# Kernel tuning notes

Measured on AMD Instinct MI355X. Metric: run time of the kernel, lower is better.

The kernel has to match this reference:

```python
import jax, jax.numpy as jnp
import numpy as np

B, S, DIM, HEADS, DHEAD = 1, 1992, 2048, 16, 128
NKI_SEQ_ALIGN = 128
EPS = 1e-6


def setup_inputs() -> dict:
    key = jax.random.key(0)
    ks = jax.random.split(key, 8)
    hidden_states = jax.random.normal(ks[0], (B, S, DIM), dtype=jnp.float32)
    # realistic rotary tables, full head_dim with interleaved pair angles
    pos = jnp.arange(S, dtype=jnp.float32)
    inv_freq = 1.0 / (10000.0 ** (jnp.arange(0, DHEAD, 2, dtype=jnp.float32) / DHEAD))
    ang = pos[:, None] * inv_freq[None, :]                      # [S, DHEAD/2]
    full = jnp.stack([ang, ang], axis=-1).reshape(S, DHEAD)     # interleave
    freqs_cos = jnp.cos(full)[None, :, None, :]                 # [1,S,1,DHEAD]
    freqs_sin = jnp.sin(full)[None, :, None, :]
    sc = 0.02
    wq = jax.random.normal(ks[1], (DIM, DIM), dtype=jnp.float32) * sc
    wk = jax.random.normal(ks[2], (DIM, DIM), dtype=jnp.float32) * sc
    wv = jax.random.normal(ks[3], (DIM, DIM), dtype=jnp.float32) * sc
    wo = jax.random.normal(ks[4], (DIM, DIM), dtype=jnp.float32) * sc
    bq = jax.random.normal(ks[5], (DIM,), dtype=jnp.float32) * sc
    bk = jax.random.normal(ks[6], (DIM,), dtype=jnp.float32) * sc
    bv = jax.random.normal(ks[7], (DIM,), dtype=jnp.float32) * sc
    bo = jnp.zeros((DIM,), dtype=jnp.float32)
    norm_q_w = jnp.ones((DIM,), dtype=jnp.float32)
    norm_k_w = jnp.ones((DIM,), dtype=jnp.float32)
    return dict(hidden_states=hidden_states, freqs_cos=freqs_cos, freqs_sin=freqs_sin,
                wq=wq, bq=bq, wk=wk, bk=bk, wv=wv, bv=bv,
                norm_q_w=norm_q_w, norm_k_w=norm_k_w, wo=wo, bo=bo)


def _rms_norm(x, weight, eps=EPS):
    xf = x.astype(jnp.float32)
    var = jnp.mean(xf * xf, axis=-1, keepdims=True)
    return (weight * (xf * jax.lax.rsqrt(var + eps))).astype(x.dtype)


def _apply_rope(x, freqs_cos, freqs_sin):
    # x: [B,H,S,D]; freqs: [1,S,1,D]
    cos = jnp.transpose(freqs_cos[..., 0::2], (0, 2, 1, 3))  # [1,1,S,D/2]
    sin = jnp.transpose(freqs_sin[..., 1::2], (0, 2, 1, 3))
    x1, x2 = x[..., 0::2], x[..., 1::2]
    o1 = x1 * cos - x2 * sin
    o2 = x1 * sin + x2 * cos
    return jnp.stack([o1, o2], axis=-1).reshape(x.shape)


def _attention_padded(q, k, v):
    # Faithful to nki_flash_attention: zero-pad seq to multiple of 128,
    # no masking of padded keys (they contribute logit 0), trim query pad.
    B_, H_, S_, D_ = q.shape
    pad = (-S_) % NKI_SEQ_ALIGN
    if pad:
        pc = [(0, 0), (0, 0), (0, pad), (0, 0)]
        q = jnp.pad(q, pc); k = jnp.pad(k, pc); v = jnp.pad(v, pc)
    scale = 1.0 / np.sqrt(D_)
    scores = jnp.einsum('bhqd,bhkd->bhqk', q, k) * scale
    probs = jax.nn.softmax(scores, axis=-1)
    out = jnp.einsum('bhqk,bhkd->bhqd', probs, v)
    return out[:, :, :S_, :]


def reference(hidden_states, freqs_cos, freqs_sin, wq, bq, wk, bk, wv, bv,
              norm_q_w, norm_k_w, wo, bo):
    b, s, _ = hidden_states.shape
    q = hidden_states @ wq.T + bq
    k = hidden_states @ wk.T + bk
    v = hidden_states @ wv.T + bv
    q = _rms_norm(q, norm_q_w)
    k = _rms_norm(k, norm_k_w)
    hd = q.shape[-1] // HEADS
    q = q.reshape(b, s, HEADS, hd).transpose(0, 2, 1, 3)
    k = k.reshape(b, s, HEADS, hd).transpose(0, 2, 1, 3)
    v = v.reshape(b, s, HEADS, hd).transpose(0, 2, 1, 3)
    q = _apply_rope(q, freqs_cos, freqs_sin)
    k = _apply_rope(k, freqs_cos, freqs_sin)
    o = _attention_padded(q, k, v)
    o = o.transpose(0, 2, 1, 3).reshape(b, s, -1)
    return o @ wo.T + bo
```

## Files before the change

kernel.cpp:

```cpp
#include <hip/hip_runtime.h>
#include <cstdint>

#define S_REAL 1992
#define S_PAD  2048
#define DIMSZ  2048
#define NHEAD  16
#define DHD    128

typedef float f32x4 __attribute__((ext_vector_type(4)));
typedef float f32x16 __attribute__((ext_vector_type(16)));
typedef __bf16 bf16x8 __attribute__((ext_vector_type(8)));
typedef unsigned short u16x8 __attribute__((ext_vector_type(8)));

__device__ __forceinline__ unsigned short f2bf(float f){
  uint32_t u = __float_as_uint(f);
  u += 0x7fffu + ((u >> 16) & 1u);
  return (unsigned short)(u >> 16);
}

__device__ __forceinline__ void gload16(const void* g, void* l){
  __builtin_amdgcn_global_load_lds(
      (const __attribute__((address_space(1))) uint32_t*)g,
      (__attribute__((address_space(3))) uint32_t*)l,
      16, 0, 0);
}

__launch_bounds__(256)
__global__ void k_cvt5(const float* __restrict__ s0, const float* __restrict__ s1,
                       const float* __restrict__ s2, const float* __restrict__ s3,
                       const float* __restrict__ s4,
                       unsigned short* __restrict__ d0, unsigned short* __restrict__ d1,
                       unsigned short* __restrict__ d2, unsigned short* __restrict__ d3,
                       unsigned short* __restrict__ d4,
                       int nX, int nW)
{
  int i = blockIdx.x * 256 + threadIdx.x;
  const float* s; unsigned short* d; int j;
  if (i < nX){ s = s0; d = d0; j = i; }
  else {
    int k = i - nX;
    int wsel = k / nW; j = k - wsel * nW;
    s = (wsel == 0) ? s1 : (wsel == 1) ? s2 : (wsel == 2) ? s3 : s4;
    d = (wsel == 0) ? d1 : (wsel == 1) ? d2 : (wsel == 2) ? d3 : d4;
  }
  const float4* sp = (const float4*)s + (size_t)j * 2;
  float4 a = sp[0], b = sp[1];
  u16x8 o;
  o[0]=f2bf(a.x); o[1]=f2bf(a.y); o[2]=f2bf(a.z); o[3]=f2bf(a.w);
  o[4]=f2bf(b.x); o[5]=f2bf(b.y); o[6]=f2bf(b.z); o[7]=f2bf(b.w);
  *((u16x8*)d + j) = o;
}

template<int BN>
__launch_bounds__(256, 2)
__global__ void k_g64(const unsigned short* __restrict__ A,
                      const unsigned short* __restrict__ B0,
                      const unsigned short* __restrict__ B1,
                      const unsigned short* __restrict__ B2,
                      const float* __restrict__ bias0,
                      const float* __restrict__ bias1,
                      const float* __restrict__ bias2,
                      float* __restrict__ C0, float* __restrict__ C1,
                      unsigned short* __restrict__ Cb,
                      int Mreal)
{
  constexpr int WN   = (BN == 128) ? 2 : 1;
  constexpr int WM   = 4 / WN;
  constexpr int MB   = (128 / WM) / 32;
  constexpr int NB   = (BN / WN) / 32;
  constexpr int AE   = 128 * 64;
  constexpr int BE   = BN * 64;
  constexpr int BUFE = AE + BE;
  constexpr int NT   = DIMSZ / 64;
  constexpr int TN   = DIMSZ / BN;
  __shared__ unsigned short lds[2 * BUFE];

  const unsigned short* Bm = (blockIdx.z == 0) ? B0 : ((blockIdx.z == 1) ? B1 : B2);
  const float* bias        = (blockIdx.z == 0) ? bias0 : ((blockIdx.z == 1) ? bias1 : bias2);
  float* C                 = (blockIdx.z == 0) ? C0 : C1;

  const int fid = blockIdx.x + gridDim.x * blockIdx.y;
  const int q   = (gridDim.x * gridDim.y) >> 3;
  const int nf  = (fid & 7) * q + (fid >> 3);
  const int m0  = (nf / TN) * 128, n0 = (nf % TN) * BN;

  const int tid = threadIdx.x;
  const int w = tid >> 6, l = tid & 63;
  const int l31 = l & 31, l5 = l >> 5;
  const int wr = (w / WN) * (128 / WM);
  const int wc = (w % WN) * (BN / WN);

  f32x16 acc[MB][NB];
  #pragma unroll
  for (int mb = 0; mb < MB; ++mb)
    #pragma unroll
    for (int nb = 0; nb < NB; ++nb)
      #pragma unroll
      for (int r = 0; r < 16; ++r) acc[mb][nb][r] = 0.f;

#define G64_STAGE(TT, PP) do{                                                     \
    const int k0s = (TT) * 64;                                                    \
    unsigned short* dst = &lds[(PP) * BUFE];                                      \
    _Pragma("unroll")                                                             \
    for (int i_ = 0; i_ < AE / 2048; ++i_){                                       \
      int lin = i_ * 256 + tid;                                                   \
      int r_ = lin >> 3, sl_ = lin & 7;                                           \
      int gr_ = m0 + r_; if (gr_ > Mreal - 1) gr_ = Mreal - 1;                    \
      gload16(A + (size_t)gr_ * DIMSZ + k0s + (sl_ ^ (r_ & 7)) * 8,               \
              dst + lin * 8);                                                     \
    }                                                                             \
    _Pragma("unroll")                                                             \
    for (int i_ = 0; i_ < BE / 2048; ++i_){                                       \
      int lin = i_ * 256 + tid;                                                   \
      int r_ = lin >> 3, sl_ = lin & 7;                                           \
      gload16(Bm + (size_t)(n0 + r_) * DIMSZ + k0s + (sl_ ^ (r_ & 7)) * 8,        \
              dst + AE + lin * 8);                                                \
    }                                                                             \
  } while(0)

#define G64_COMPUTE(PP) do{                                                       \
    const unsigned short* sb = &lds[(PP) * BUFE];                                 \
    bf16x8 a_[MB][4], b_[NB][4];                                                  \
    _Pragma("unroll")                                                             \
    for (int mb = 0; mb < MB; ++mb)                                               \
      _Pragma("unroll")                                                           \
      for (int ks = 0; ks < 4; ++ks){                                             \
        int r_ = wr + mb * 32 + l31;                                              \
        int c_ = (ks * 2 + l5) ^ (r_ & 7);                                        \
        a_[mb][ks] = *(const bf16x8*)(sb + r_ * 64 + c_ * 8);                     \
      }                                                                           \
    _Pragma("unroll")                                                             \
    for (int nb = 0; nb < NB; ++nb)                                               \
      _Pragma("unroll")                                                           \
      for (int ks = 0; ks < 4; ++ks){                                             \
        int r_ = wc + nb * 32 + l31;                                              \
        int c_ = (ks * 2 + l5) ^ (r_ & 7);                                        \
        b_[nb][ks] = *(const bf16x8*)(sb + AE + r_ * 64 + c_ * 8);                \
      }                                                                           \
    __builtin_amdgcn_s_setprio(1);                                                \
    _Pragma("unroll")                                                             \
    for (int ks = 0; ks < 4; ++ks)                                                \
      _Pragma("unroll")                                                           \
      for (int mb = 0; mb < MB; ++mb)                                             \
        _Pragma("unroll")                                                         \
        for (int nb = 0; nb < NB; ++nb)                                           \
          acc[mb][nb] = __builtin_amdgcn_mfma_f32_32x32x16_bf16(a_[mb][ks],       \
                            b_[nb][ks], acc[mb][nb], 0, 0, 0);                    \
    __builtin_amdgcn_s_setprio(0);                                                \
  } while(0)

  G64_STAGE(0, 0);
  asm volatile("s_waitcnt vmcnt(0)" ::: "memory");
  __builtin_amdgcn_s_barrier();
  int p = 0;
  for (int tt = 0; tt < NT; ++tt){
    if (tt + 1 < NT) G64_STAGE(tt + 1, p ^ 1);
    G64_COMPUTE(p);
    asm volatile("s_waitcnt vmcnt(0)" ::: "memory");
    __builtin_amdgcn_s_barrier();
    p ^= 1;
  }
#undef G64_STAGE
#undef G64_COMPUTE

  const bool vout = (blockIdx.z == 2);
  #pragma unroll
  for (int nb = 0; nb < NB; ++nb){
    int col = n0 + wc + nb * 32 + l31;
    float bz = bias[col];
    #pragma unroll
    for (int mb = 0; mb < MB; ++mb){
      #pragma unroll
      for (int r = 0; r < 16; ++r){
        int row = m0 + wr + mb * 32 + (r & 3) + 8 * (r >> 2) + 4 * l5;
        if (row < Mreal){
          if (vout) Cb[(size_t)row * DIMSZ + col] = f2bf(acc[mb][nb][r] + bz);
          else      C[(size_t)row * DIMSZ + col] = acc[mb][nb][r] + bz;
        }
      }
    }
  }
}

__launch_bounds__(256)
__global__ void k_normrope2(const float* __restrict__ Qf, const float* __restrict__ Kf,
                            const float* __restrict__ nqw, const float* __restrict__ nkw,
                            const float* __restrict__ fc, const float* __restrict__ fs,
                            unsigned short* __restrict__ OutQ, unsigned short* __restrict__ OutK)
{
  const int s = blockIdx.x;
  const int isK = blockIdx.y;
  const float* Xf = isK ? Kf : Qf;
  const float* nw = isK ? nkw : nqw;
  unsigned short* Out = isK ? OutK : OutQ;
  const float scale = isK ? 1.0f : (0.08838834764831843f * 1.4426950408889634f);
  const int swz = isK;

  const int t = threadIdx.x;
  const int w = t >> 6, l = t & 63;
  __shared__ float wred[4];
  float v[8];
  float ss = 0.f;
  if (s < S_REAL){
    const float4* p = (const float4*)(Xf + (size_t)s * DIMSZ) + t * 2;
    float4 a = p[0], b = p[1];
    v[0]=a.x; v[1]=a.y; v[2]=a.z; v[3]=a.w; v[4]=b.x; v[5]=b.y; v[6]=b.z; v[7]=b.w;
    #pragma unroll
    for (int j = 0; j < 8; ++j) ss += v[j] * v[j];
  }
  #pragma unroll
  for (int off = 32; off >= 1; off >>= 1) ss += __shfl_xor(ss, off);
  if (l == 0) wred[w] = ss;
  __syncthreads();
  float tot = wred[0] + wred[1] + wred[2] + wred[3];
  float rinv = rsqrtf(tot * (1.f / DIMSZ) + 1e-6f);

  const int h  = t >> 4;
  const int d0 = (t & 15) * 8;
  const int b  = t & 15;
  const int bsw = swz ? (b ^ (s & 7)) : b;
  unsigned short* dst = Out + ((size_t)h * S_PAD + s) * DHD + bsw * 8;
  u16x8 o;
  if (s < S_REAL){
    #pragma unroll
    for (int i = 0; i < 4; ++i){
      float c_ = fc[s * DHD + d0 + 2 * i];
      float s_ = fs[s * DHD + d0 + 2 * i + 1];
      float x1 = v[2 * i]     * rinv * nw[t * 8 + 2 * i];
      float x2 = v[2 * i + 1] * rinv * nw[t * 8 + 2 * i + 1];
      o[2 * i]     = f2bf((x1 * c_ - x2 * s_) * scale);
      o[2 * i + 1] = f2bf((x1 * s_ + x2 * c_) * scale);
    }
  } else {
    #pragma unroll
    for (int j = 0; j < 8; ++j) o[j] = 0;
  }
  *(u16x8*)dst = o;
}

__launch_bounds__(256)
__global__ void k_vtrans(const unsigned short* __restrict__ Vb, unsigned short* __restrict__ Vth)
{
  __shared__ unsigned short tile[64][72];
  const int t = threadIdx.x;
  const int s0 = blockIdx.x * 64, c0 = blockIdx.y * 64;
  #pragma unroll
  for (int i = 0; i < 2; ++i){
    int lin = i * 256 + t;
    int r = lin >> 3, ck = lin & 7;
    u16x8 val = (u16x8){0,0,0,0,0,0,0,0};
    if (s0 + r < S_REAL)
      val = *(const u16x8*)(Vb + (size_t)(s0 + r) * DIMSZ + c0 + ck * 8);
    *(u16x8*)&tile[r][ck * 8] = val;
  }
  __syncthreads();
  const int cl = t >> 2;
  const int cc = c0 + cl;
  #pragma unroll
  for (int bi = 0; bi < 2; ++bi){
    int b = (t & 3) * 2 + bi;
    u16x8 o;
    #pragma unroll
    for (int j = 0; j < 8; ++j) o[j] = tile[b * 8 + j][cl];
    int bsw = b ^ (cc & 7);
    *(u16x8*)(Vth + (size_t)cc * S_PAD + s0 + bsw * 8) = o;
  }
}

__launch_bounds__(512)
__global__ void k_attn(const unsigned short* __restrict__ Qh,
                       const unsigned short* __restrict__ Kh,
                       const unsigned short* __restrict__ Vth,
                       unsigned short* __restrict__ O)
{
  __shared__ unsigned short kbuf[3][64 * 128];
  __shared__ unsigned short vbuf[4][128 * 64];
  __shared__ unsigned short pbuf[8][16 * 64];
  const int flat = blockIdx.x + gridDim.x * blockIdx.y;
  const int h  = (flat & 7) * 2 + ((flat >> 3) & 1);
  const int q0 = (flat >> 4) * 128;
  const int t = threadIdx.x, w = t >> 6, l = t & 63;
  const int lr = l & 15, lg = l >> 4;

  const unsigned short* Qp = Qh + ((size_t)h * S_PAD + q0 + w * 16 + lr) * DHD;
  bf16x8 qf[4];
  #pragma unroll
  for (int ks = 0; ks < 4; ++ks) qf[ks] = *(const bf16x8*)(Qp + ks * 32 + lg * 8);

  f32x4 acc[8];
  #pragma unroll
  for (int nf = 0; nf < 8; ++nf) acc[nf] = (f32x4){0.f, 0.f, 0.f, 0.f};
  float m = -3.0e38f, lsum = 0.f;

#define ATT_STAGE(KT, BK_, BV_) do{                                                 \
    _Pragma("unroll")                                                               \
    for (int i_ = 0; i_ < 2; ++i_){                                                 \
      int lin = i_ * 512 + t;                                                       \
      int rK = lin >> 4, ckK = lin & 15;                                            \
      gload16(Kh + ((size_t)h * S_PAD + (KT) * 64 + rK) * DHD + ckK * 8,            \
              &kbuf[BK_][lin * 8]);                                                 \
    }                                                                               \
    _Pragma("unroll")                                                               \
    for (int i_ = 0; i_ < 2; ++i_){                                                 \
      int lin = i_ * 512 + t;                                                       \
      int rV = lin >> 3, ckV = lin & 7;                                             \
      gload16(Vth + ((size_t)h * DHD + rV) * S_PAD + (KT) * 64 + ckV * 8,           \
              &vbuf[BV_][lin * 8]);                                                 \
    }                                                                               \
  } while(0)

#define SM_PV(SF, VB) do{                                                           \
    float pmax = SF[0][0];                                                          \
    _Pragma("unroll")                                                               \
    for (int kvf = 0; kvf < 4; ++kvf)                                               \
      _Pragma("unroll")                                                             \
      for (int j = 0; j < 4; ++j) pmax = fmaxf(pmax, SF[kvf][j]);                   \
    pmax = fmaxf(pmax, __shfl_xor(pmax, 16));                                       \
    pmax = fmaxf(pmax, __shfl_xor(pmax, 32));                                       \
    float fr = 1.f;                                                                 \
    if (!__all(pmax - m <= 8.0f)){                                                  \
      float mn = fmaxf(m, pmax);                                                    \
      fr = exp2f(m - mn);                                                           \
      m = mn;                                                                       \
      float fv0 = __shfl(fr, lg * 4 + 0);                                           \
      float fv1 = __shfl(fr, lg * 4 + 1);                                           \
      float fv2 = __shfl(fr, lg * 4 + 2);                                           \
      float fv3 = __shfl(fr, lg * 4 + 3);                                           \
      f32x4 fv = (f32x4){fv0, fv1, fv2, fv3};                                       \
      _Pragma("unroll")                                                             \
      for (int nf = 0; nf < 8; ++nf) acc[nf] *= fv;                                 \
    }                                                                               \
    float p_[4][4];                                                                 \
    float psum = 0.f;                                                               \
    _Pragma("unroll")                                                               \
    for (int kvf = 0; kvf < 4; ++kvf)                                               \
      _Pragma("unroll")                                                             \
      for (int j = 0; j < 4; ++j){ p_[kvf][j] = exp2f(SF[kvf][j] - m); psum += p_[kvf][j]; } \
    lsum = lsum * fr + psum;                                                        \
    char* pb = (char*)pbuf[w];                                                      \
    _Pragma("unroll")                                                               \
    for (int kvf = 0; kvf < 4; ++kvf){                                              \
      uint2 wv;                                                                     \
      wv.x = (uint32_t)f2bf(p_[kvf][0]) | ((uint32_t)f2bf(p_[kvf][1]) << 16);       \
      wv.y = (uint32_t)f2bf(p_[kvf][2]) | ((uint32_t)f2bf(p_[kvf][3]) << 16);       \
      int byte = lr * 128 + (((kvf * 2 + (lg >> 1)) ^ (lr & 7)) * 16) + (lg & 1) * 8;\
      *(uint2*)(pb + byte) = wv;                                                    \
    }                                                                               \
    bf16x8 pf[2];                                                                   \
    _Pragma("unroll")                                                               \
    for (int c = 0; c < 2; ++c)                                                     \
      pf[c] = *(const bf16x8*)(pb + lr * 128 + ((c * 4 + lg) ^ (lr & 7)) * 16);     \
    __builtin_amdgcn_s_setprio(1);                                                  \
    _Pragma("unroll")                                                               \
    for (int nf = 0; nf < 8; ++nf){                                                 \
      int cc = nf * 16 + lr;                                                        \
      _Pragma("unroll")                                                             \
      for (int ks = 0; ks < 2; ++ks){                                               \
        int blk = (ks * 4 + lg) ^ (cc & 7);                                         \
        bf16x8 vf = *(const bf16x8*)&vbuf[VB][cc * 64 + blk * 8];                   \
        acc[nf] = __builtin_amdgcn_mfma_f32_16x16x32_bf16(pf[ks], vf, acc[nf], 0, 0, 0); \
      }                                                                             \
    }                                                                               \
    __builtin_amdgcn_s_setprio(0);                                                  \
  } while(0)

  ATT_STAGE(0, 0, 0);
  ATT_STAGE(1, 1, 1);
  asm volatile("s_waitcnt vmcnt(4)" ::: "memory");
  __builtin_amdgcn_s_barrier();

  constexpr int NKT = S_PAD / 64;
  f32x4 sfp[4];
  int kb = 0, sk = 2, sv = 2, vp = 3;
  for (int kt = 0; kt < NKT; ++kt){
    if (kt < NKT - 2) ATT_STAGE(kt + 2, sk, sv);

    f32x4 sfc[4];
    __builtin_amdgcn_s_setprio(1);
    #pragma unroll
    for (int kvf = 0; kvf < 4; ++kvf){
      sfc[kvf] = (f32x4){0.f, 0.f, 0.f, 0.f};
      int r = kvf * 16 + lr;
      #pragma unroll
      for (int ks = 0; ks < 4; ++ks){
        int blk = (ks * 4 + lg) ^ (r & 7);
        bf16x8 kf = *(const bf16x8*)&kbuf[kb][r * 128 + blk * 8];
        sfc[kvf] = __builtin_amdgcn_mfma_f32_16x16x32_bf16(kf, qf[ks], sfc[kvf], 0, 0, 0);
      }
    }
    __builtin_amdgcn_s_setprio(0);

    if (kt > 0) SM_PV(sfp, vp);

    #pragma unroll
    for (int kvf = 0; kvf < 4; ++kvf) sfp[kvf] = sfc[kvf];

    if (kt < NKT - 2)       asm volatile("s_waitcnt vmcnt(4)" ::: "memory");
    else if (kt == NKT - 2) asm volatile("s_waitcnt vmcnt(0)" ::: "memory");
    if (kt < NKT - 1) __builtin_amdgcn_s_barrier();

    kb = (kb == 2) ? 0 : kb + 1;
    sk = (sk == 2) ? 0 : sk + 1;
    sv = (sv == 3) ? 0 : sv + 1;
    vp = (vp == 3) ? 0 : vp + 1;
  }
  SM_PV(sfp, vp);
#undef ATT_STAGE
#undef SM_PV

  lsum += __shfl_xor(lsum, 16);
  lsum += __shfl_xor(lsum, 32);
  float ls0 = __shfl(lsum, lg * 4 + 0);
  float ls1 = __shfl(lsum, lg * 4 + 1);
  float ls2 = __shfl(lsum, lg * 4 + 2);
  float ls3 = __shfl(lsum, lg * 4 + 3);
  f32x4 lsv = (f32x4){1.f / ls0, 1.f / ls1, 1.f / ls2, 1.f / ls3};

  #pragma unroll
  for (int nf = 0; nf < 8; ++nf){
    #pragma unroll
    for (int j = 0; j < 4; ++j){
      int row = q0 + w * 16 + lg * 4 + j;
      if (row < S_REAL)
        O[(size_t)row * DIMSZ + h * DHD + nf * 16 + lr] = f2bf(acc[nf][j] * lsv[j]);
    }
  }
}

extern "C" void kernel_launch(void* const* d_in, const int* in_sizes, int n_in,
                              void* d_out, int out_size, void* d_ws, size_t ws_size,
                              hipStream_t stream)
{
  const float* hidden = (const float*)d_in[0];
  const float* fc  = (const float*)d_in[1];
  const float* fs  = (const float*)d_in[2];
  const float* wq  = (const float*)d_in[3];
  const float* bq  = (const float*)d_in[4];
  const float* wk  = (const float*)d_in[5];
  const float* bk  = (const float*)d_in[6];
  const float* wv  = (const float*)d_in[7];
  const float* bv  = (const float*)d_in[8];
  const float* nqw = (const float*)d_in[9];
  const float* nkw = (const float*)d_in[10];
  const float* wo  = (const float*)d_in[11];
  const float* bo  = (const float*)d_in[12];
  float* out = (float*)d_out;

  char* ws = (char*)d_ws;
  size_t off = 0;
  auto alloc = [&](size_t bytes) -> void* {
    void* p = ws + off;
    off += (bytes + 255) & ~(size_t)255;
    return p;
  };
  unsigned short* Xb  = (unsigned short*)alloc((size_t)S_REAL * DIMSZ * 2);
  unsigned short* Wqb = (unsigned short*)alloc((size_t)DIMSZ * DIMSZ * 2);
  unsigned short* Wkb = (unsigned short*)alloc((size_t)DIMSZ * DIMSZ * 2);
  unsigned short* Wvb = (unsigned short*)alloc((size_t)DIMSZ * DIMSZ * 2);
  unsigned short* Wob = (unsigned short*)alloc((size_t)DIMSZ * DIMSZ * 2);
  float* Qf = (float*)alloc((size_t)S_REAL * DIMSZ * 4);
  float* Kf = (float*)alloc((size_t)S_REAL * DIMSZ * 4);
  unsigned short* Vb  = (unsigned short*)alloc((size_t)S_REAL * DIMSZ * 2);
  unsigned short* Qhh = (unsigned short*)alloc((size_t)NHEAD * S_PAD * DHD * 2);
  unsigned short* Khh = (unsigned short*)alloc((size_t)NHEAD * S_PAD * DHD * 2);
  unsigned short* Vth = (unsigned short*)alloc((size_t)NHEAD * DHD * S_PAD * 2);
  unsigned short* Oa  = (unsigned short*)alloc((size_t)S_REAL * DIMSZ * 2);

  {
    int nX = S_REAL * DIMSZ / 8;
    int nW = DIMSZ * DIMSZ / 8;
    int total = nX + 4 * nW;
    k_cvt5<<<total / 256, 256, 0, stream>>>(hidden, wq, wk, wv, wo,
                                            Xb, Wqb, Wkb, Wvb, Wob, nX, nW);
  }

  k_g64<128><<<dim3(16, 16, 3), 256, 0, stream>>>(Xb, Wqb, Wkb, Wvb, bq, bk, bv,
                                                  Qf, Kf, Vb, S_REAL);

  k_normrope2<<<dim3(S_PAD, 2), 256, 0, stream>>>(Qf, Kf, nqw, nkw, fc, fs, Qhh, Khh);

  k_vtrans<<<dim3(S_PAD / 64, DIMSZ / 64), 256, 0, stream>>>(Vb, Vth);

  k_attn<<<dim3(S_PAD / 128, NHEAD), 512, 0, stream>>>(Qhh, Khh, Vth, Oa);

  k_g64<64><<<dim3(16, 32, 1), 256, 0, stream>>>(Oa, Wob, Wob, Wob, bo, bo, bo,
                                                 out, out, nullptr, S_REAL);
}
```

Measured before the change: 233.8 us.

## Switch GEMMs to triple-buffered K=32 pipeline and store Q/K as bf16

Replaces the double-buffered K=64 GEMM with a triple-buffered K=32 kernel that keeps two tile loads in flight. It waits with vmcnt(4) so the next stage's loads overlap compute, and the smaller LDS footprint allows three blocks per CU. Q and K projections are now written as bf16 instead of fp32, which halves the intermediate traffic read by the norm/rope kernel at some precision cost before RMS norm. The output projection now uses 128x128 tiles with 256 blocks instead of 128x64 tiles with 512.

```diff
diff --git a/kernel.cpp b/kernel.cpp
--- a/kernel.cpp
+++ b/kernel.cpp
@@ -18,11 +18,20 @@
   return (unsigned short)(u >> 16);
 }
 
+__device__ __forceinline__ float bf2f(unsigned short b){
+  return __uint_as_float((uint32_t)b << 16);
+}
+
 __device__ __forceinline__ void gload16(const void* g, void* l){
   __builtin_amdgcn_global_load_lds(
       (const __attribute__((address_space(1))) uint32_t*)g,
       (__attribute__((address_space(3))) uint32_t*)l,
       16, 0, 0);
+}
+
+template<int N> __device__ __forceinline__ void waitbar(){
+  if constexpr (N == 4) asm volatile("s_waitcnt vmcnt(4)\n\ts_barrier" ::: "memory");
+  else                  asm volatile("s_waitcnt vmcnt(0)\n\ts_barrier" ::: "memory");
 }
 
 __launch_bounds__(256)
@@ -51,131 +60,128 @@
   *((u16x8*)d + j) = o;
 }
 
-template<int BN>
-__launch_bounds__(256, 2)
-__global__ void k_g64(const unsigned short* __restrict__ A,
+__launch_bounds__(256, 3)
+__global__ void k_g32(const unsigned short* __restrict__ A,
                       const unsigned short* __restrict__ B0,
                       const unsigned short* __restrict__ B1,
                       const unsigned short* __restrict__ B2,
                       const float* __restrict__ bias0,
                       const float* __restrict__ bias1,
                       const float* __restrict__ bias2,
-                      float* __restrict__ C0, float* __restrict__ C1,
-                      unsigned short* __restrict__ Cb,
-                      int Mreal)
-{
-  constexpr int WN   = (BN == 128) ? 2 : 1;
-  constexpr int WM   = 4 / WN;
-  constexpr int MB   = (128 / WM) / 32;
-  constexpr int NB   = (BN / WN) / 32;
-  constexpr int AE   = 128 * 64;
-  constexpr int BE   = BN * 64;
-  constexpr int BUFE = AE + BE;
-  constexpr int NT   = DIMSZ / 64;
-  constexpr int TN   = DIMSZ / BN;
-  __shared__ unsigned short lds[2 * BUFE];
+                      float* __restrict__ C0,
+                      unsigned short* __restrict__ Cb0,
+                      unsigned short* __restrict__ Cb1,
+                      unsigned short* __restrict__ Cb2,
+                      int bf16_out, int Mreal)
+{
+  constexpr int BUFE = 8192;
+  constexpr int NT   = DIMSZ / 32;
+  __shared__ unsigned short lds[3 * BUFE];
 
   const unsigned short* Bm = (blockIdx.z == 0) ? B0 : ((blockIdx.z == 1) ? B1 : B2);
   const float* bias        = (blockIdx.z == 0) ? bias0 : ((blockIdx.z == 1) ? bias1 : bias2);
-  float* C                 = (blockIdx.z == 0) ? C0 : C1;
+  unsigned short* Cbm      = (blockIdx.z == 0) ? Cb0 : ((blockIdx.z == 1) ? Cb1 : Cb2);
 
   const int fid = blockIdx.x + gridDim.x * blockIdx.y;
   const int q   = (gridDim.x * gridDim.y) >> 3;
   const int nf  = (fid & 7) * q + (fid >> 3);
-  const int m0  = (nf / TN) * 128, n0 = (nf % TN) * BN;
+  const int m0  = (nf >> 4) * 128, n0 = (nf & 15) * 128;
 
   const int tid = threadIdx.x;
   const int w = tid >> 6, l = tid & 63;
   const int l31 = l & 31, l5 = l >> 5;
-  const int wr = (w / WN) * (128 / WM);
-  const int wc = (w % WN) * (BN / WN);
-
-  f32x16 acc[MB][NB];
-  #pragma unroll
-  for (int mb = 0; mb < MB; ++mb)
-    #pragma unroll
-    for (int nb = 0; nb < NB; ++nb)
+  const int wr = (w >> 1) * 64, wc = (w & 1) * 64;
+
+  f32x16 acc[2][2];
+  #pragma unroll
+  for (int mb = 0; mb < 2; ++mb)
+    #pragma unroll
+    for (int nb = 0; nb < 2; ++nb)
       #pragma unroll
       for (int r = 0; r < 16; ++r) acc[mb][nb][r] = 0.f;
 
-#define G64_STAGE(TT, PP) do{                                                     \
-    const int k0s = (TT) * 64;                                                    \
-    unsigned short* dst = &lds[(PP) * BUFE];                                      \
+#define G32_STAGE(TT, BASE) do{                                                   \
+    const int k0s = (TT) * 32;                                                    \
+    unsigned short* dst = (BASE);                                                 \
     _Pragma("unroll")                                                             \
-    for (int i_ = 0; i_ < AE / 2048; ++i_){                                       \
+    for (int i_ = 0; i_ < 2; ++i_){                                               \
       int lin = i_ * 256 + tid;                                                   \
-      int r_ = lin >> 3, sl_ = lin & 7;                                           \
+      int r_ = lin >> 2, pos_ = lin & 3;                                          \
       int gr_ = m0 + r_; if (gr_ > Mreal - 1) gr_ = Mreal - 1;                    \
-      gload16(A + (size_t)gr_ * DIMSZ + k0s + (sl_ ^ (r_ & 7)) * 8,               \
+      gload16(A + (size_t)gr_ * DIMSZ + k0s + (pos_ ^ ((r_ >> 1) & 3)) * 8,       \
               dst + lin * 8);                                                     \
     }                                                                             \
     _Pragma("unroll")                                                             \
-    for (int i_ = 0; i_ < BE / 2048; ++i_){                                       \
+    for (int i_ = 0; i_ < 2; ++i_){                                               \
       int lin = i_ * 256 + tid;                                                   \
-      int r_ = lin >> 3, sl_ = lin & 7;                                           \
-      gload16(Bm + (size_t)(n0 + r_) * DIMSZ + k0s + (sl_ ^ (r_ & 7)) * 8,        \
-              dst + AE + lin * 8);                                                \
+      int r_ = lin >> 2, pos_ = lin & 3;                                          \
+      gload16(Bm + (size_t)(n0 + r_) * DIMSZ + k0s + (pos_ ^ ((r_ >> 1) & 3)) * 8,\
+              dst + 4096 + lin * 8);                                              \
     }                                                                             \
   } while(0)
 
-#define G64_COMPUTE(PP) do{                                                       \
-    const unsigned short* sb = &lds[(PP) * BUFE];                                 \
-    bf16x8 a_[MB][4], b_[NB][4];                                                  \
+#define G32_COMPUTE(BASE) do{                                                     \
+    const unsigned short* sb = (BASE);                                            \
+    bf16x8 a_[2][2], b_[2][2];                                                    \
     _Pragma("unroll")                                                             \
-    for (int mb = 0; mb < MB; ++mb)                                               \
+    for (int mb = 0; mb < 2; ++mb)                                                \
       _Pragma("unroll")                                                           \
-      for (int ks = 0; ks < 4; ++ks){                                             \
+      for (int ks = 0; ks < 2; ++ks){                                             \
         int r_ = wr + mb * 32 + l31;                                              \
-        int c_ = (ks * 2 + l5) ^ (r_ & 7);                                        \
-        a_[mb][ks] = *(const bf16x8*)(sb + r_ * 64 + c_ * 8);                     \
+        int c_ = (ks * 2 + l5) ^ ((r_ >> 1) & 3);                                 \
+        a_[mb][ks] = *(const bf16x8*)(sb + r_ * 32 + c_ * 8);                     \
       }                                                                           \
     _Pragma("unroll")                                                             \
-    for (int nb = 0; nb < NB; ++nb)                                               \
+    for (int nb = 0; nb < 2; ++nb)                                                \
       _Pragma("unroll")                                                           \
-      for (int ks = 0; ks < 4; ++ks){                                             \
+      for (int ks = 0; ks < 2; ++ks){                                             \
         int r_ = wc + nb * 32 + l31;                                              \
-        int c_ = (ks * 2 + l5) ^ (r_ & 7);                                        \
-        b_[nb][ks] = *(const bf16x8*)(sb + AE + r_ * 64 + c_ * 8);                \
+        int c_ = (ks * 2 + l5) ^ ((r_ >> 1) & 3);                                 \
+        b_[nb][ks] = *(const bf16x8*)(sb + 4096 + r_ * 32 + c_ * 8);              \
       }                                                                           \
     __builtin_amdgcn_s_setprio(1);                                                \
     _Pragma("unroll")                                                             \
-    for (int ks = 0; ks < 4; ++ks)                                                \
+    for (int ks = 0; ks < 2; ++ks)                                                \
       _Pragma("unroll")                                                           \
-      for (int mb = 0; mb < MB; ++mb)                                             \
+      for (int mb = 0; mb < 2; ++mb)                                              \
         _Pragma("unroll")                                                         \
-        for (int nb = 0; nb < NB; ++nb)                                           \
+        for (int nb = 0; nb < 2; ++nb)                                            \
           acc[mb][nb] = __builtin_amdgcn_mfma_f32_32x32x16_bf16(a_[mb][ks],       \
                             b_[nb][ks], acc[mb][nb], 0, 0, 0);                    \
     __builtin_amdgcn_s_setprio(0);                                                \
   } while(0)
 
-  G64_STAGE(0, 0);
-  asm volatile("s_waitcnt vmcnt(0)" ::: "memory");
-  __builtin_amdgcn_s_barrier();
-  int p = 0;
-  for (int tt = 0; tt < NT; ++tt){
-    if (tt + 1 < NT) G64_STAGE(tt + 1, p ^ 1);
-    G64_COMPUTE(p);
-    asm volatile("s_waitcnt vmcnt(0)" ::: "memory");
-    __builtin_amdgcn_s_barrier();
-    p ^= 1;
-  }
-#undef G64_STAGE
-#undef G64_COMPUTE
-
-  const bool vout = (blockIdx.z == 2);
-  #pragma unroll
-  for (int nb = 0; nb < NB; ++nb){
+  G32_STAGE(0, lds);
+  G32_STAGE(1, lds + BUFE);
+  int bc = 0, bs = 2;
+  for (int tt = 0; tt < NT - 2; ++tt){
+    waitbar<4>();
+    G32_STAGE(tt + 2, lds + bs * BUFE);
+    G32_COMPUTE(lds + bc * BUFE);
+    bs = (bs == 2) ? 0 : bs + 1;
+    bc = (bc == 2) ? 0 : bc + 1;
+  }
+  waitbar<4>();
+  G32_COMPUTE(lds + bc * BUFE);
+  bc = (bc == 2) ? 0 : bc + 1;
+  waitbar<0>();
+  G32_COMPUTE(lds + bc * BUFE);
+
+#undef G32_STAGE
+#undef G32_COMPUTE
+
+  #pragma unroll
+  for (int nb = 0; nb < 2; ++nb){
     int col = n0 + wc + nb * 32 + l31;
     float bz = bias[col];
     #pragma unroll
-    for (int mb = 0; mb < MB; ++mb){
+    for (int mb = 0; mb < 2; ++mb){
       #pragma unroll
       for (int r = 0; r < 16; ++r){
         int row = m0 + wr + mb * 32 + (r & 3) + 8 * (r >> 2) + 4 * l5;
         if (row < Mreal){
-          if (vout) Cb[(size_t)row * DIMSZ + col] = f2bf(acc[mb][nb][r] + bz);
-          else      C[(size_t)row * DIMSZ + col] = acc[mb][nb][r] + bz;
+          if (bf16_out) Cbm[(size_t)row * DIMSZ + col] = f2bf(acc[mb][nb][r] + bz);
+          else          C0[(size_t)row * DIMSZ + col] = acc[mb][nb][r] + bz;
         }
       }
     }
@@ -183,14 +189,15 @@
 }
 
 __launch_bounds__(256)
-__global__ void k_normrope2(const float* __restrict__ Qf, const float* __restrict__ Kf,
+__global__ void k_normrope2(const unsigned short* __restrict__ Qb,
+                            const unsigned short* __restrict__ Kb,
                             const float* __restrict__ nqw, const float* __restrict__ nkw,
                             const float* __restrict__ fc, const float* __restrict__ fs,
                             unsigned short* __restrict__ OutQ, unsigned short* __restrict__ OutK)
 {
   const int s = blockIdx.x;
   const int isK = blockIdx.y;
-  const float* Xf = isK ? Kf : Qf;
+  const unsigned short* Xb = isK ? Kb : Qb;
   const float* nw = isK ? nkw : nqw;
   unsigned short* Out = isK ? OutK : OutQ;
   const float scale = isK ? 1.0f : (0.08838834764831843f * 1.4426950408889634f);
@@ -202,11 +209,9 @@
   float v[8];
   float ss = 0.f;
   if (s < S_REAL){
-    const float4* p = (const float4*)(Xf + (size_t)s * DIMSZ) + t * 2;
-    float4 a = p[0], b = p[1];
-    v[0]=a.x; v[1]=a.y; v[2]=a.z; v[3]=a.w; v[4]=b.x; v[5]=b.y; v[6]=b.z; v[7]=b.w;
-    #pragma unroll
-    for (int j = 0; j < 8; ++j) ss += v[j] * v[j];
+    u16x8 raw = *((const u16x8*)(Xb + (size_t)s * DIMSZ) + t);
+    #pragma unroll
+    for (int j = 0; j < 8; ++j){ v[j] = bf2f(raw[j]); ss += v[j] * v[j]; }
   }
   #pragma unroll
   for (int off = 32; off >= 1; off >>= 1) ss += __shfl_xor(ss, off);
@@ -458,8 +463,8 @@
   unsigned short* Wkb = (unsigned short*)alloc((size_t)DIMSZ * DIMSZ * 2);
   unsigned short* Wvb = (unsigned short*)alloc((size_t)DIMSZ * DIMSZ * 2);
   unsigned short* Wob = (unsigned short*)alloc((size_t)DIMSZ * DIMSZ * 2);
-  float* Qf = (float*)alloc((size_t)S_REAL * DIMSZ * 4);
-  float* Kf = (float*)alloc((size_t)S_REAL * DIMSZ * 4);
+  unsigned short* Qb  = (unsigned short*)alloc((size_t)S_REAL * DIMSZ * 2);
+  unsigned short* Kb  = (unsigned short*)alloc((size_t)S_REAL * DIMSZ * 2);
   unsigned short* Vb  = (unsigned short*)alloc((size_t)S_REAL * DIMSZ * 2);
   unsigned short* Qhh = (unsigned short*)alloc((size_t)NHEAD * S_PAD * DHD * 2);
   unsigned short* Khh = (unsigned short*)alloc((size_t)NHEAD * S_PAD * DHD * 2);
@@ -474,15 +479,15 @@
                                             Xb, Wqb, Wkb, Wvb, Wob, nX, nW);
   }
 
-  k_g64<128><<<dim3(16, 16, 3), 256, 0, stream>>>(Xb, Wqb, Wkb, Wvb, bq, bk, bv,
-                                                  Qf, Kf, Vb, S_REAL);
-
-  k_normrope2<<<dim3(S_PAD, 2), 256, 0, stream>>>(Qf, Kf, nqw, nkw, fc, fs, Qhh, Khh);
+  k_g32<<<dim3(16, 16, 3), 256, 0, stream>>>(Xb, Wqb, Wkb, Wvb, bq, bk, bv,
+                                             nullptr, Qb, Kb, Vb, 1, S_REAL);
+
+  k_normrope2<<<dim3(S_PAD, 2), 256, 0, stream>>>(Qb, Kb, nqw, nkw, fc, fs, Qhh, Khh);
 
   k_vtrans<<<dim3(S_PAD / 64, DIMSZ / 64), 256, 0, stream>>>(Vb, Vth);
 
   k_attn<<<dim3(S_PAD / 128, NHEAD), 512, 0, stream>>>(Qhh, Khh, Vth, Oa);
 
-  k_g64<64><<<dim3(16, 32, 1), 256, 0, stream>>>(Oa, Wob, Wob, Wob, bo, bo, bo,
-                                                 out, out, nullptr, S_REAL);
-}
+  k_g32<<<dim3(16, 16, 1), 256, 0, stream>>>(Oa, Wob, Wob, Wob, bo, bo, bo,
+                                             out, nullptr, nullptr, nullptr, 0, S_REAL);
+}
```

Measured after the change: 226.5 us. -3.1%, faster.
